# Kernel tuning notes

Hardware: AMD Instinct MI355X
Metric: run time of the kernel (lower is better)

Reference implementation:

```python
import jax, jax.numpy as jnp
import numpy as np

BATCH, T, N = 8, 2048, 512


def setup_inputs() -> dict:
    key = jax.random.key(0)
    ks = jax.random.split(key, 8)
    scale = 1.0 / np.sqrt(2.0 * (N + N) / 2.0) / np.sqrt(2.0)  # GlorotNormal / sqrt(2)
    u = jax.random.normal(ks[0], (BATCH, T, N), dtype=jnp.float32)
    C_re = jax.random.normal(ks[1], (N, N), dtype=jnp.float32) * scale
    C_im = jax.random.normal(ks[2], (N, N), dtype=jnp.float32) * scale
    B_re = jax.random.normal(ks[3], (N, N), dtype=jnp.float32) * scale
    B_im = jax.random.normal(ks[4], (N, N), dtype=jnp.float32) * scale
    D = jax.random.normal(ks[5], (N,), dtype=jnp.float32)
    # nu drawn from the numerically-stable end of [log(-log rmax), log(-log rmin)]
    nu = jax.random.uniform(ks[6], (N,), minval=-4.6, maxval=-3.7, dtype=jnp.float32)
    theta = jax.random.uniform(ks[7], (N,), minval=0.0, maxval=3.14 / 10, dtype=jnp.float32)
    # gamma initialized as sqrt(1 - |lambda|^2), lambda = exp(-exp(nu) + i*theta)
    gamma = jnp.sqrt(1.0 - jnp.exp(-2.0 * jnp.exp(nu)))
    return {"u": u, "C_re": C_re, "C_im": C_im, "B_re": B_re, "B_im": B_im,
            "D": D, "nu": nu, "theta": theta, "gamma": gamma}


def reference(u, C_re, C_im, B_re, B_im, D, nu, theta, gamma):
    # log_lambda = -exp(nu) + i*theta  (the TF code names this `lambda_`)
    log_lam = (-jnp.exp(nu)).astype(jnp.complex64) + 1j * theta.astype(jnp.complex64)  # (n,)
    t = jnp.arange(u.shape[1], dtype=jnp.float32).astype(jnp.complex64)[:, None]       # (T,1)
    lam_pow = jnp.exp(log_lam[None, :] * t)    # (T,n) == diag(Lambda^t)
    lam_minpow = jnp.exp(-log_lam[None, :] * t)  # (T,n) == diag(Lambda^-t)
    Bm = (B_re + 1j * B_im).astype(jnp.complex64)  # (n,n)
    Cm = (C_re + 1j * C_im).astype(jnp.complex64)  # (n,n)
    # new_u = (gamma * u) @ B   (complex)
    new_u = (gamma * u).astype(jnp.complex64) @ Bm  # (b,t,n)
    # diag einsums in the original are elementwise multiplies
    x = jnp.cumsum(new_u * lam_minpow[None], axis=1) * lam_pow[None]  # (b,t,n)
    y = jnp.real(x @ Cm) + D * u
    return y
```

## Files before the change

### kernel.cpp

```cpp
#include <hip/hip_runtime.h>
#include <hip/hip_bf16.h>
#include <math.h>
#include <stdint.h>

#define BATCH 8
#define T_LEN 2048
#define NDIM 512
#define M_ROWS (BATCH * T_LEN)
#define CHUNK 32
#define NCHUNK (T_LEN / CHUNK)


typedef __attribute__((ext_vector_type(8))) short bf16x8;
typedef __attribute__((ext_vector_type(4))) float floatx4;

#define VMWAIT(n) asm volatile("s_waitcnt vmcnt(" #n ")" ::: "memory")

__device__ __forceinline__ unsigned short f2bf(float f) {
    union { float f; unsigned u; } v; v.f = f;
    unsigned r = v.u + 0x7fff + ((v.u >> 16) & 1);
    return (unsigned short)(r >> 16);
}
__device__ __forceinline__ float bf2f(unsigned short h) {
    union { unsigned u; float f; } v; v.u = ((unsigned)h) << 16;
    return v.f;
}
__device__ __forceinline__ float bf2f_lo(unsigned u) {
    union { unsigned u; float f; } v; v.u = u << 16; return v.f;
}
__device__ __forceinline__ float bf2f_hi(unsigned u) {
    union { unsigned u; float f; } v; v.u = u & 0xffff0000u; return v.f;
}

__device__ __forceinline__ void gld_lds16(const unsigned short* g, unsigned short* l) {
    __builtin_amdgcn_global_load_lds(
        (const __attribute__((address_space(1))) unsigned int*)(uintptr_t)g,
        (__attribute__((address_space(3))) unsigned int*)(uintptr_t)l,
        16, 0, 0);
}

__global__ __launch_bounds__(256) void k_prep(
    const float* __restrict__ u,
    const float* __restrict__ Bre, const float* __restrict__ Bim,
    const float* __restrict__ Cre, const float* __restrict__ Cim,
    const float* __restrict__ gamma,
    unsigned short* __restrict__ ubf,
    unsigned short* __restrict__ BT, unsigned short* __restrict__ CT)
{
    __shared__ unsigned short tile[32][33];
    const int blk = blockIdx.x;
    if (blk < 4096) {
        size_t i = ((size_t)blk * 256 + threadIdx.x) * 8;
        float4 a = *(const float4*)&u[i];
        float4 b = *(const float4*)&u[i + 4];
        ushort4 p0, p1;
        p0.x = f2bf(a.x); p0.y = f2bf(a.y); p0.z = f2bf(a.z); p0.w = f2bf(a.w);
        p1.x = f2bf(b.x); p1.y = f2bf(b.y); p1.z = f2bf(b.z); p1.w = f2bf(b.w);
        *(ushort4*)&ubf[i] = p0;
        *(ushort4*)&ubf[i + 4] = p1;
        return;
    }
    const int p = blk - 4096;
    const int z = p >> 8;
    const int rem = p & 255;
    const int n0 = (rem & 15) * 32, k0 = (rem >> 4) * 32;
    const float* __restrict__ src = (z == 0) ? Bre : (z == 1) ? Bim : (z == 2) ? Cre : Cim;
    const int tx = threadIdx.x & 31, ty = threadIdx.x >> 5;

#pragma unroll
    for (int j = 0; j < 4; ++j) {
        int k = k0 + ty + j * 8;
        float s = (z < 2) ? gamma[k] : (z == 3 ? -1.f : 1.f);
        tile[ty + j * 8][tx] = f2bf(s * src[(size_t)k * NDIM + n0 + tx]);
    }
    __syncthreads();
#pragma unroll
    for (int j = 0; j < 4; ++j) {
        int n = n0 + ty + j * 8;
        unsigned short v = tile[tx][ty + j * 8];
        if (z == 0) {
            int row = ((n >> 6) << 7) + (n & 63);
            BT[(size_t)row * 512 + k0 + tx] = v;
        } else if (z == 1) {
            int row = ((n >> 6) << 7) + 64 + (n & 63);
            BT[(size_t)row * 512 + k0 + tx] = v;
        } else if (z == 2) {
            int k = k0 + tx;
            int col = ((k >> 6) << 7) + (k & 63);
            CT[(size_t)n * 1024 + col] = v;
        } else {
            int k = k0 + tx;
            int col = ((k >> 6) << 7) + 64 + (k & 63);
            CT[(size_t)n * 1024 + col] = v;
        }
    }
}

__global__ __launch_bounds__(512) void k_gemm_in(
    const unsigned short* __restrict__ A,
    const unsigned short* __restrict__ BT,
    const float* __restrict__ nu, const float* __restrict__ theta,
    unsigned short* __restrict__ X,
    float* __restrict__ carry)
{
    __shared__ unsigned short smem[65536];

    const int tid = threadIdx.x;
    const int w = tid >> 6, l = tid & 63;
    const int bm = blockIdx.x * 256;
    const int bn = blockIdx.y * 256;
    const int wm = (w & 1) * 128, wn = (w >> 1) * 64;
    const int lm = l & 15, lq = l >> 4;
    const int sr = tid >> 3;
    const int scw = ((tid & 7) ^ (sr & 7)) * 8;
    const int scl = (tid & 7) * 8;
    const int rsw = (lm & 7) << 3;

    floatx4 acc[8][4];
#pragma unroll
    for (int i = 0; i < 8; ++i)
#pragma unroll
        for (int j = 0; j < 4; ++j) acc[i][j] = (floatx4)0.f;

    auto SPAIR = [&](int buf, int t, int pair) {
        unsigned short* as = &smem[buf * 32768];
        unsigned short* bs = as + 16384;
        const int k0 = t * 64;
        if (pair == 0) {
            gld_lds16(&BT[(size_t)(bn + 0 * 64 + sr) * 512 + k0 + scw], &bs[(0 * 64 + sr) * 64 + scl]);
            gld_lds16(&BT[(size_t)(bn + 1 * 64 + sr) * 512 + k0 + scw], &bs[(1 * 64 + sr) * 64 + scl]);
        } else if (pair == 1) {
            gld_lds16(&BT[(size_t)(bn + 2 * 64 + sr) * 512 + k0 + scw], &bs[(2 * 64 + sr) * 64 + scl]);
            gld_lds16(&BT[(size_t)(bn + 3 * 64 + sr) * 512 + k0 + scw], &bs[(3 * 64 + sr) * 64 + scl]);
        } else if (pair == 2) {
            gld_lds16(&A[(size_t)(bm + 0 * 64 + sr) * 512 + k0 + scw], &as[(0 * 64 + sr) * 64 + scl]);
            gld_lds16(&A[(size_t)(bm + 2 * 64 + sr) * 512 + k0 + scw], &as[(2 * 64 + sr) * 64 + scl]);
        } else {
            gld_lds16(&A[(size_t)(bm + 1 * 64 + sr) * 512 + k0 + scw], &as[(1 * 64 + sr) * 64 + scl]);
            gld_lds16(&A[(size_t)(bm + 3 * 64 + sr) * 512 + k0 + scw], &as[(3 * 64 + sr) * 64 + scl]);
        }
    };

    auto PHASE = [&](int buf, int qa, int qb, int stt, int pair) {
        const unsigned short* as = &smem[buf * 32768];
        const unsigned short* bs = as + 16384;
        bf16x8 af[4][2], bfr[2][2];
#pragma unroll
        for (int i4 = 0; i4 < 4; ++i4)
#pragma unroll
            for (int ks = 0; ks < 2; ++ks)
                af[i4][ks] = *(const bf16x8*)&as[(wm + (qa * 4 + i4) * 16 + lm) * 64 + ((ks * 32 + lq * 8) ^ rsw)];
#pragma unroll
        for (int j2 = 0; j2 < 2; ++j2)
#pragma unroll
            for (int ks = 0; ks < 2; ++ks)
                bfr[j2][ks] = *(const bf16x8*)&bs[(wn + (qb * 2 + j2) * 16 + lm) * 64 + ((ks * 32 + lq * 8) ^ rsw)];
        if (pair >= 0) SPAIR(buf ^ 1, stt, pair);
        __builtin_amdgcn_s_setprio(1);
#pragma unroll
        for (int i4 = 0; i4 < 4; ++i4)
#pragma unroll
            for (int j2 = 0; j2 < 2; ++j2)
#pragma unroll
                for (int ks = 0; ks < 2; ++ks)
                    acc[qa * 4 + i4][qb * 2 + j2] = __builtin_amdgcn_mfma_f32_16x16x32_bf16(
                        af[i4][ks], bfr[j2][ks], acc[qa * 4 + i4][qb * 2 + j2], 0, 0, 0);
        __builtin_amdgcn_s_setprio(0);
    };

    SPAIR(0, 0, 0); SPAIR(0, 0, 1); SPAIR(0, 0, 2); SPAIR(0, 0, 3);
    VMWAIT(2);
    __builtin_amdgcn_s_barrier();
    __builtin_amdgcn_sched_barrier(0);

#pragma unroll
    for (int t = 0; t < 8; ++t) {
        const int ct = t & 1;
        const bool st = (t < 7);
        PHASE(ct, 0, 0, t + 1, st ? 0 : -1);
        PHASE(ct, 0, 1, t + 1, st ? 1 : -1);
        if (st) { VMWAIT(4); } else { VMWAIT(0); }
        __builtin_amdgcn_s_barrier();
        __builtin_amdgcn_sched_barrier(0);
        PHASE(ct, 1, 0, t + 1, st ? 2 : -1);
        PHASE(ct, 1, 1, t + 1, st ? 3 : -1);
        if (st) {
            VMWAIT(2);
            __builtin_amdgcn_s_barrier();
            __builtin_amdgcn_sched_barrier(0);
        }
    }

    __syncthreads();
#pragma unroll
    for (int i = 0; i < 8; ++i)
#pragma unroll
        for (int j = 0; j < 4; ++j) {
            int lcol = wn + j * 16 + lm;
#pragma unroll
            for (int r = 0; r < 4; ++r) {
                int lrow = wm + i * 16 + lq * 4 + r;
                unsigned short v = f2bf(acc[i][j][r]);
                smem[lrow * 256 + lcol] = v;
                X[(size_t)(bm + lrow) * 1024 + bn + lcol] = v;
            }
        }
    __syncthreads();
#pragma unroll
    for (int q = 0; q < 2; ++q) {
        const int s = tid + q * 512;
        const int chunk = s >> 7;
        const int ch = s & 127;
        const int n = (bn >> 1) + ch;
        const int gl = ch >> 6, cc = ch & 63;
        const int recol = gl * 128 + cc;
        const float rr = __expf(-__expf(nu[n]));
        const float lre = rr * __cosf(theta[n]);
        const float lim = rr * __sinf(theta[n]);
        const unsigned short* base = &smem[chunk * 32 * 256 + recol];
        float xre = 0.f, xim = 0.f;
#pragma unroll 8
        for (int t = 0; t < 32; ++t) {
            float ure = bf2f(base[t * 256]);
            float uim = bf2f(base[t * 256 + 64]);
            float a = lre * xre - lim * xim + ure;
            float b = lre * xim + lim * xre + uim;
            xre = a; xim = b;
        }
        const int bb = bm >> 11;
        const int cg = ((bm & 2047) >> 5) + chunk;
        size_t ci = ((size_t)bb * NCHUNK + cg) * NDIM + n;
        *(float2*)&carry[ci * 2] = make_float2(xre, xim);
    }
}

__global__ __launch_bounds__(512) void k_scan_gemm(
    const unsigned short* __restrict__ X,
    const unsigned short* __restrict__ CT,
    const float* __restrict__ nu, const float* __restrict__ theta,
    const float* __restrict__ carry,
    const float* __restrict__ D,
    const unsigned short* __restrict__ Ubf,
    float* __restrict__ Y)
{
    __shared__ unsigned short Asm[32 * 1024];
    __shared__ unsigned short Bsm[2][512 * 32];

    const int tid = threadIdx.x;
    const int c = blockIdx.x, b = blockIdx.y;
    const int m0 = b * T_LEN + c * CHUNK;

    const int brow4 = tid >> 2;
    const int bslot = tid & 3;
    auto SB = [&](int buf, int t) {
        const int k0 = t * 32;
#pragma unroll
        for (int o = 0; o < 4; ++o) {
            int row = o * 128 + brow4;
            gld_lds16(&CT[(size_t)row * 1024 + k0 + ((bslot ^ (row & 3)) * 8)],
                      &Bsm[buf][row * 32 + bslot * 8]);
        }
    };

    SB(0, 0);
    SB(1, 1);

    const int n = tid;
    const float ex = __expf(nu[n]);
    const float r0 = __expf(-ex);
    const float lre = r0 * __cosf(theta[n]);
    const float lim = r0 * __sinf(theta[n]);
    const float rc = expf(-ex * (float)CHUNK);
    const float th = theta[n] * (float)CHUNK;
    const float A0 = rc * cosf(th), B0 = rc * sinf(th);
    float xre = 0.f, xim = 0.f;
    for (int cc = 0; cc < c; ++cc) {
        float2 cv = *(const float2*)&carry[(((size_t)b * NCHUNK + cc) * NDIM + n) * 2];
        float a  = A0 * xre - B0 * xim + cv.x;
        float b2 = A0 * xim + B0 * xre + cv.y;
        xre = a; xim = b2;
    }

    const int recol = ((n >> 6) << 7) + (n & 63);
#pragma unroll 8
    for (int t = 0; t < 32; ++t) {
        size_t m = (size_t)(m0 + t) * 1024;
        float ure = bf2f(X[m + recol]);
        float uim = bf2f(X[m + recol + 64]);
        float a  = lre * xre - lim * xim + ure;
        float b2 = lre * xim + lim * xre + uim;
        xre = a; xim = b2;
        const int sw = (t & 7) << 3;
        Asm[t * 1024 + (recol ^ sw)] = f2bf(xre);
        Asm[t * 1024 + ((recol + 64) ^ sw)] = f2bf(xim);
    }

    __syncthreads();

    const int w = tid >> 6, l = tid & 63;
    const int wn = w * 64;
    const int lm = l & 15, lq = l >> 4;
    const int asw = (lm & 7) << 3;
    const int bsw = (lm & 3) << 3;

    floatx4 acc[2][4];
#pragma unroll
    for (int mi = 0; mi < 2; ++mi)
#pragma unroll
        for (int j = 0; j < 4; ++j) acc[mi][j] = (floatx4)0.f;

    auto COMPUTE = [&](int buf, int t) {
        const int k0 = t * 32;
        bf16x8 af[2], bfr[4];
#pragma unroll
        for (int mi = 0; mi < 2; ++mi)
            af[mi] = *(const bf16x8*)&Asm[(mi * 16 + lm) * 1024 + ((k0 + lq * 8) ^ asw)];
#pragma unroll
        for (int j = 0; j < 4; ++j)
            bfr[j] = *(const bf16x8*)&Bsm[buf][(wn + j * 16 + lm) * 32 + ((lq * 8) ^ bsw)];
        __builtin_amdgcn_s_setprio(1);
#pragma unroll
        for (int mi = 0; mi < 2; ++mi)
#pragma unroll
            for (int j = 0; j < 4; ++j)
                acc[mi][j] = __builtin_amdgcn_mfma_f32_16x16x32_bf16(af[mi], bfr[j], acc[mi][j], 0, 0, 0);
        __builtin_amdgcn_s_setprio(0);
    };

#pragma unroll 4
    for (int t = 0; t < 32; ++t) {
        if (t < 31) { VMWAIT(4); } else { VMWAIT(0); }
        __builtin_amdgcn_s_barrier();
        __builtin_amdgcn_sched_barrier(0);
        COMPUTE(t & 1, t);
        __builtin_amdgcn_s_barrier();
        __builtin_amdgcn_sched_barrier(0);
        if (t < 30) SB(t & 1, t + 2);
    }

#pragma unroll
    for (int mi = 0; mi < 2; ++mi)
#pragma unroll
        for (int j = 0; j < 4; ++j) {
            int col = wn + j * 16 + lm;
            float dv = D[col];
#pragma unroll
            for (int r = 0; r < 4; ++r) {
                int row = mi * 16 + lq * 4 + r;
                size_t off = (size_t)(m0 + row) * NDIM + col;
                Y[off] = acc[mi][j][r] + dv * bf2f(Ubf[off]);
            }
        }
}

extern "C" void kernel_launch(void* const* d_in, const int* in_sizes, int n_in,
                              void* d_out, int out_size, void* d_ws, size_t ws_size,
                              hipStream_t stream)
{
    const float* u     = (const float*)d_in[0];
    const float* C_re  = (const float*)d_in[1];
    const float* C_im  = (const float*)d_in[2];
    const float* B_re  = (const float*)d_in[3];
    const float* B_im  = (const float*)d_in[4];
    const float* D     = (const float*)d_in[5];
    const float* nu    = (const float*)d_in[6];
    const float* theta = (const float*)d_in[7];
    const float* gamma = (const float*)d_in[8];
    float* y = (float*)d_out;

    unsigned short* X   = (unsigned short*)d_ws;
    unsigned short* ubf = X + (size_t)M_ROWS * 1024;
    unsigned short* BT  = ubf + (size_t)M_ROWS * 512;
    unsigned short* CT  = BT + (size_t)1024 * 512;
    float* carry = (float*)(CT + (size_t)512 * 1024);

    k_prep<<<4096 + 1024, 256, 0, stream>>>(u, B_re, B_im, C_re, C_im, gamma, ubf, BT, CT);
    k_gemm_in<<<dim3(M_ROWS / 256, 4), 512, 0, stream>>>(ubf, BT, nu, theta, X, carry);
    k_scan_gemm<<<dim3(NCHUNK, BATCH), 512, 0, stream>>>(X, CT, nu, theta, carry, D, ubf, y);
}
```

Baseline: 196.5 us.

## Retile output scan-GEMM into 256x128 tiles with per-K-group in-block scan

Replaces the per-chunk output kernel, where each block covered 32 time rows by all 512 output columns, with 256-row by 128-column tiles. Each block rebuilds the scanned state for its K-slice in 64-channel groups, using chunk prefixes kept in shared memory. This gives more MFMA work per loaded C tile and better reuse of the B operand. The cost is that each block redoes the scan for its K groups four times, once per column tile, and the pipeline now synchronises once per group instead of double-buffering per K step.

```diff
diff --git a/kernel.cpp b/kernel.cpp
--- a/kernel.cpp
+++ b/kernel.cpp
@@ -24,12 +24,6 @@
 __device__ __forceinline__ float bf2f(unsigned short h) {
     union { unsigned u; float f; } v; v.u = ((unsigned)h) << 16;
     return v.f;
-}
-__device__ __forceinline__ float bf2f_lo(unsigned u) {
-    union { unsigned u; float f; } v; v.u = u << 16; return v.f;
-}
-__device__ __forceinline__ float bf2f_hi(unsigned u) {
-    union { unsigned u; float f; } v; v.u = u & 0xffff0000u; return v.f;
 }
 
 __device__ __forceinline__ void gld_lds16(const unsigned short* g, unsigned short* l) {
@@ -234,7 +228,7 @@
     }
 }
 
-__global__ __launch_bounds__(512) void k_scan_gemm(
+__global__ __launch_bounds__(512) void k_gemm_out(
     const unsigned short* __restrict__ X,
     const unsigned short* __restrict__ CT,
     const float* __restrict__ nu, const float* __restrict__ theta,
@@ -243,112 +237,139 @@
     const unsigned short* __restrict__ Ubf,
     float* __restrict__ Y)
 {
-    __shared__ unsigned short Asm[32 * 1024];
-    __shared__ unsigned short Bsm[2][512 * 32];
+    __shared__ unsigned short Asm[256 * 128];
+    __shared__ unsigned short Bsm[2][128 * 64];
+    __shared__ float2 Pref[8][512];
+    __shared__ float2 Lam[512];
 
     const int tid = threadIdx.x;
-    const int c = blockIdx.x, b = blockIdx.y;
-    const int m0 = b * T_LEN + c * CHUNK;
-
-    const int brow4 = tid >> 2;
-    const int bslot = tid & 3;
+    const int bm = blockIdx.x * 256;
+    const int bn = blockIdx.y * 128;
+    const int bb = bm >> 11;
+    const int cg0 = (bm & 2047) >> 5;
+
     auto SB = [&](int buf, int t) {
-        const int k0 = t * 32;
-#pragma unroll
-        for (int o = 0; o < 4; ++o) {
-            int row = o * 128 + brow4;
-            gld_lds16(&CT[(size_t)row * 1024 + k0 + ((bslot ^ (row & 3)) * 8)],
-                      &Bsm[buf][row * 32 + bslot * 8]);
+        const int row = tid >> 3;
+        const int slot = tid & 7;
+        const int k0 = t * 64;
+#pragma unroll
+        for (int o = 0; o < 2; ++o) {
+            int r = o * 64 + row;
+            gld_lds16(&CT[(size_t)(bn + r) * 1024 + k0 + ((slot ^ (r & 7)) * 8)],
+                      &Bsm[buf][r * 64 + slot * 8]);
         }
     };
 
     SB(0, 0);
     SB(1, 1);
 
-    const int n = tid;
-    const float ex = __expf(nu[n]);
-    const float r0 = __expf(-ex);
-    const float lre = r0 * __cosf(theta[n]);
-    const float lim = r0 * __sinf(theta[n]);
-    const float rc = expf(-ex * (float)CHUNK);
-    const float th = theta[n] * (float)CHUNK;
-    const float A0 = rc * cosf(th), B0 = rc * sinf(th);
-    float xre = 0.f, xim = 0.f;
-    for (int cc = 0; cc < c; ++cc) {
-        float2 cv = *(const float2*)&carry[(((size_t)b * NCHUNK + cc) * NDIM + n) * 2];
-        float a  = A0 * xre - B0 * xim + cv.x;
-        float b2 = A0 * xim + B0 * xre + cv.y;
-        xre = a; xim = b2;
-    }
-
-    const int recol = ((n >> 6) << 7) + (n & 63);
+    {
+        const int n = tid;
+        const float ex = __expf(nu[n]);
+        const float rr = __expf(-ex);
+        const float lre = rr * __cosf(theta[n]);
+        const float lim = rr * __sinf(theta[n]);
+        Lam[n] = make_float2(lre, lim);
+        const float rc = expf(-ex * (float)CHUNK);
+        const float th = theta[n] * (float)CHUNK;
+        const float A0 = rc * cosf(th), B0 = rc * sinf(th);
+        float pre_re = 0.f, pre_im = 0.f;
+        for (int cc = 0; cc < cg0; ++cc) {
+            float2 cv = *(const float2*)&carry[(((size_t)bb * NCHUNK + cc) * NDIM + n) * 2];
+            float a = A0 * pre_re - B0 * pre_im + cv.x;
+            float b = A0 * pre_im + B0 * pre_re + cv.y;
+            pre_re = a; pre_im = b;
+        }
+#pragma unroll
+        for (int ck = 0; ck < 8; ++ck) {
+            Pref[ck][n] = make_float2(pre_re, pre_im);
+            float2 cv = *(const float2*)&carry[(((size_t)bb * NCHUNK + cg0 + ck) * NDIM + n) * 2];
+            float a = A0 * pre_re - B0 * pre_im + cv.x;
+            float b = A0 * pre_im + B0 * pre_re + cv.y;
+            pre_re = a; pre_im = b;
+        }
+    }
+
+    const int wv = tid >> 6, l = tid & 63;
+    const int wm = (wv & 3) * 64, wn = (wv >> 2) * 64;
+    const int lm = l & 15, lq = l >> 4;
+    const int sch = tid & 63;
+    const int schunk = tid >> 6;
+
+    floatx4 acc[4][4];
+#pragma unroll
+    for (int i = 0; i < 4; ++i)
+#pragma unroll
+        for (int j = 0; j < 4; ++j) acc[i][j] = (floatx4)0.f;
+
+    __syncthreads();
+
+    for (int g = 0; g < 8; ++g) {
+        {
+            const int n2 = g * 64 + sch;
+            const float2 lam = Lam[n2];
+            const float2 P = Pref[schunk][n2];
+            float sre = P.x, sim = P.y;
+            const unsigned short* xr = &X[(size_t)(bm + schunk * 32) * 1024 + g * 128 + sch];
+            unsigned short* arow = &Asm[(schunk * 32) * 128 + (sch & 7)];
+            const int sre_slot = sch >> 3;
 #pragma unroll 8
-    for (int t = 0; t < 32; ++t) {
-        size_t m = (size_t)(m0 + t) * 1024;
-        float ure = bf2f(X[m + recol]);
-        float uim = bf2f(X[m + recol + 64]);
-        float a  = lre * xre - lim * xim + ure;
-        float b2 = lre * xim + lim * xre + uim;
-        xre = a; xim = b2;
-        const int sw = (t & 7) << 3;
-        Asm[t * 1024 + (recol ^ sw)] = f2bf(xre);
-        Asm[t * 1024 + ((recol + 64) ^ sw)] = f2bf(xim);
-    }
-
-    __syncthreads();
-
-    const int w = tid >> 6, l = tid & 63;
-    const int wn = w * 64;
-    const int lm = l & 15, lq = l >> 4;
-    const int asw = (lm & 7) << 3;
-    const int bsw = (lm & 3) << 3;
-
-    floatx4 acc[2][4];
-#pragma unroll
-    for (int mi = 0; mi < 2; ++mi)
-#pragma unroll
-        for (int j = 0; j < 4; ++j) acc[mi][j] = (floatx4)0.f;
-
-    auto COMPUTE = [&](int buf, int t) {
-        const int k0 = t * 32;
-        bf16x8 af[2], bfr[4];
-#pragma unroll
-        for (int mi = 0; mi < 2; ++mi)
-            af[mi] = *(const bf16x8*)&Asm[(mi * 16 + lm) * 1024 + ((k0 + lq * 8) ^ asw)];
-#pragma unroll
-        for (int j = 0; j < 4; ++j)
-            bfr[j] = *(const bf16x8*)&Bsm[buf][(wn + j * 16 + lm) * 32 + ((lq * 8) ^ bsw)];
-        __builtin_amdgcn_s_setprio(1);
-#pragma unroll
-        for (int mi = 0; mi < 2; ++mi)
+            for (int t = 0; t < 32; ++t) {
+                float ure = bf2f(xr[(size_t)t * 1024]);
+                float uim = bf2f(xr[(size_t)t * 1024 + 64]);
+                float a = lam.x * sre - lam.y * sim + ure;
+                float b = lam.x * sim + lam.y * sre + uim;
+                sre = a; sim = b;
+                const int sw = t & 7;
+                arow[t * 128 + ((sre_slot ^ sw) * 8)] = f2bf(sre);
+                arow[t * 128 + (((8 + sre_slot) ^ sw) * 8)] = f2bf(sim);
+            }
+        }
+        __syncthreads();
+
+#pragma unroll
+        for (int ktl = 0; ktl < 2; ++ktl) {
+            bf16x8 af[4][2], bfr[4][2];
+#pragma unroll
+            for (int i = 0; i < 4; ++i)
+#pragma unroll
+                for (int ks = 0; ks < 2; ++ks) {
+                    int row = wm + i * 16 + lm;
+                    af[i][ks] = *(const bf16x8*)&Asm[row * 128 + (((ktl * 8 + ks * 4 + lq) ^ (lm & 7)) * 8)];
+                }
 #pragma unroll
             for (int j = 0; j < 4; ++j)
-                acc[mi][j] = __builtin_amdgcn_mfma_f32_16x16x32_bf16(af[mi], bfr[j], acc[mi][j], 0, 0, 0);
-        __builtin_amdgcn_s_setprio(0);
-    };
-
-#pragma unroll 4
-    for (int t = 0; t < 32; ++t) {
-        if (t < 31) { VMWAIT(4); } else { VMWAIT(0); }
-        __builtin_amdgcn_s_barrier();
-        __builtin_amdgcn_sched_barrier(0);
-        COMPUTE(t & 1, t);
-        __builtin_amdgcn_s_barrier();
-        __builtin_amdgcn_sched_barrier(0);
-        if (t < 30) SB(t & 1, t + 2);
-    }
-
-#pragma unroll
-    for (int mi = 0; mi < 2; ++mi)
+#pragma unroll
+                for (int ks = 0; ks < 2; ++ks) {
+                    int row = wn + j * 16 + lm;
+                    bfr[j][ks] = *(const bf16x8*)&Bsm[ktl][row * 64 + (((ks * 4 + lq) ^ (lm & 7)) * 8)];
+                }
+            __builtin_amdgcn_s_setprio(1);
+#pragma unroll
+            for (int i = 0; i < 4; ++i)
+#pragma unroll
+                for (int j = 0; j < 4; ++j)
+#pragma unroll
+                    for (int ks = 0; ks < 2; ++ks)
+                        acc[i][j] = __builtin_amdgcn_mfma_f32_16x16x32_bf16(
+                            af[i][ks], bfr[j][ks], acc[i][j], 0, 0, 0);
+            __builtin_amdgcn_s_setprio(0);
+        }
+        __syncthreads();
+        if (g < 7) { SB(0, 2 * g + 2); SB(1, 2 * g + 3); }
+    }
+
+#pragma unroll
+    for (int i = 0; i < 4; ++i)
 #pragma unroll
         for (int j = 0; j < 4; ++j) {
-            int col = wn + j * 16 + lm;
+            int col = bn + wn + j * 16 + lm;
             float dv = D[col];
 #pragma unroll
             for (int r = 0; r < 4; ++r) {
-                int row = mi * 16 + lq * 4 + r;
-                size_t off = (size_t)(m0 + row) * NDIM + col;
-                Y[off] = acc[mi][j][r] + dv * bf2f(Ubf[off]);
+                int row = bm + wm + i * 16 + lq * 4 + r;
+                size_t off = (size_t)row * NDIM + col;
+                Y[off] = acc[i][j][r] + dv * bf2f(Ubf[off]);
             }
         }
 }
@@ -376,5 +397,5 @@
 
     k_prep<<<4096 + 1024, 256, 0, stream>>>(u, B_re, B_im, C_re, C_im, gamma, ubf, BT, CT);
     k_gemm_in<<<dim3(M_ROWS / 256, 4), 512, 0, stream>>>(ubf, BT, nu, theta, X, carry);
-    k_scan_gemm<<<dim3(NCHUNK, BATCH), 512, 0, stream>>>(X, CT, nu, theta, carry, D, ubf, y);
-}
+    k_gemm_out<<<dim3(M_ROWS / 256, 4), 512, 0, stream>>>(X, CT, nu, theta, carry, D, ubf, y);
+}
```

After: 177.1 us. 9.9% less time.
